# Kernel tuning notes

Hardware: AMD Instinct MI355X
Metric: run time of the kernel (lower is better)

The kernel has to match this reference:

```python
import jax, jax.numpy as jnp
import numpy as np

B, S, E, H = 2, 2048, 1024, 16
HD = E // H


def setup_inputs() -> dict:
    key = jax.random.key(0)
    ks = jax.random.split(key, 5)
    scale = 0.02
    return {
        "x": jax.random.normal(ks[0], (B, S, E), dtype=jnp.float32),
        "qkv_w": jax.random.normal(ks[1], (3 * E, E), dtype=jnp.float32) * scale,
        "qkv_b": jax.random.normal(ks[2], (3 * E,), dtype=jnp.float32) * scale,
        "out_w": jax.random.normal(ks[3], (E, E), dtype=jnp.float32) * scale,
        "out_b": jax.random.normal(ks[4], (E,), dtype=jnp.float32) * scale,
    }


def reference(x, qkv_w, qkv_b, out_w, out_b):
    b, s, e = x.shape
    scale = 1.0 / jnp.sqrt(jnp.float32(HD))
    # fused QKV projection: torch Linear is x @ W.T + b
    qkv = x @ qkv_w.T + qkv_b                       # [b, s, 3e]
    qkv = qkv.reshape(b, s, 3, H, HD)
    qkv = jnp.transpose(qkv, (2, 0, 3, 1, 4))       # [3, b, h, s, hd]
    q, k, v = qkv[0], qkv[1], qkv[2]
    scores = jnp.einsum('bhqd,bhkd->bhqk', q, k) * scale
    # causal mask (atmask=True): mask strictly upper triangle
    causal = jnp.triu(jnp.ones((s, s), dtype=bool), k=1)
    scores = jnp.where(causal, -jnp.inf, scores)
    attn = jax.nn.softmax(scores, axis=-1)          # dropout p=0.0 -> identity
    out = jnp.einsum('bhqk,bhkd->bhqd', attn, v)    # [b, h, s, hd]
    out = jnp.transpose(out, (0, 2, 1, 3)).reshape(b, s, e)
    return out @ out_w.T + out_b
```

## Files before the change

### kernel.cpp

```cpp
#include <hip/hip_runtime.h>
#include <cmath>

typedef __attribute__((ext_vector_type(8))) __bf16 bf16x8;
typedef __attribute__((ext_vector_type(8))) unsigned short ushort8v;
typedef __attribute__((ext_vector_type(4))) float f32x4;

__device__ inline unsigned short f2bf(float f) {
    unsigned int u = __float_as_uint(f);
    unsigned int r = (u + 0x7fffu + ((u >> 16) & 1u)) >> 16;
    return (unsigned short)r;
}

__device__ inline bf16x8 ld8(const unsigned short* p) {
    uint4 v = *(const uint4*)p;
    return __builtin_bit_cast(bf16x8, v);
}

__device__ inline f32x4 mfma16(bf16x8 a, bf16x8 b, f32x4 c) {
    return __builtin_amdgcn_mfma_f32_16x16x32_bf16(a, b, c, 0, 0, 0);
}

__device__ inline unsigned pk2t(float a, float b) {
    return __builtin_amdgcn_perm(__float_as_uint(b), __float_as_uint(a), 0x07060302u);
}

__device__ inline void gl_lds16(const unsigned short* g, const unsigned short* l) {
    __builtin_amdgcn_global_load_lds(
        (const __attribute__((address_space(1))) void*)(unsigned long long)g,
        (__attribute__((address_space(3))) void*)(unsigned)(unsigned long long)l,
        16, 0, 0);
}

#define NX4  1048576
#define NW14 786432
#define NW24 262144
__global__ __launch_bounds__(256) void cvt3(const float* __restrict__ x,
                                            const float* __restrict__ w1,
                                            const float* __restrict__ w2,
                                            unsigned short* __restrict__ xb,
                                            unsigned short* __restrict__ w1b,
                                            unsigned short* __restrict__ w2b) {
    int i = blockIdx.x * 256 + threadIdx.x;
    const float* src;
    unsigned short* dst;
    int off;
    if (i < NX4)              { src = x;  dst = xb;  off = i; }
    else if (i < NX4 + NW14)  { src = w1; dst = w1b; off = i - NX4; }
    else                      { src = w2; dst = w2b; off = i - NX4 - NW14; }
    float4 v = ((const float4*)src)[off];
    ushort4 o;
    o.x = f2bf(v.x); o.y = f2bf(v.y); o.z = f2bf(v.z); o.w = f2bf(v.w);
    ((ushort4*)dst)[off] = o;
}

__global__ __launch_bounds__(256) void gemm_out(const unsigned short* __restrict__ A,
                                                const unsigned short* __restrict__ B,
                                                const float* __restrict__ bias,
                                                float* __restrict__ C,
                                                int M, int N, int K) {
    __shared__ __align__(16) unsigned short As0[64 * 32];
    __shared__ __align__(16) unsigned short Bs0[128 * 32];
    __shared__ __align__(16) unsigned short As1[64 * 32];
    __shared__ __align__(16) unsigned short Bs1[128 * 32];
    const int m0 = blockIdx.y * 64;
    const int n0 = blockIdx.x * 128;
    const int t = threadIdx.x;
    const int wave = t >> 6, lane = t & 63;
    const int l16 = lane & 15, quad = lane >> 4;
    const int wm = (wave >> 1) * 32, wn = (wave & 1) * 64;

    f32x4 acc[2][4] = {};

    const int ra = t >> 2, ka = (t & 3) * 8;
    const int b1 = 256 + t;
    const int rb0 = t >> 2, kb0 = (t & 3) * 8;
    const int rb1 = b1 >> 2, kb1 = (b1 & 3) * 8;

    for (int k0 = 0; k0 < K; k0 += 64) {
        __syncthreads();
        gl_lds16(A + (size_t)(m0 + ra) * K + k0 + ka,        As0 + t * 8);
        gl_lds16(B + (size_t)(n0 + rb0) * K + k0 + kb0,      Bs0 + t * 8);
        gl_lds16(B + (size_t)(n0 + rb1) * K + k0 + kb1,      Bs0 + b1 * 8);
        gl_lds16(A + (size_t)(m0 + ra) * K + k0 + 32 + ka,   As1 + t * 8);
        gl_lds16(B + (size_t)(n0 + rb0) * K + k0 + 32 + kb0, Bs1 + t * 8);
        gl_lds16(B + (size_t)(n0 + rb1) * K + k0 + 32 + kb1, Bs1 + b1 * 8);
        __syncthreads();

        bf16x8 af[2], bfr[4];
        #pragma unroll
        for (int i = 0; i < 2; ++i)
            af[i] = ld8(As0 + (wm + i * 16 + l16) * 32 + quad * 8);
        #pragma unroll
        for (int j = 0; j < 4; ++j)
            bfr[j] = ld8(Bs0 + (wn + j * 16 + l16) * 32 + quad * 8);
        #pragma unroll
        for (int i = 0; i < 2; ++i)
            #pragma unroll
            for (int j = 0; j < 4; ++j)
                acc[i][j] = mfma16(af[i], bfr[j], acc[i][j]);

        #pragma unroll
        for (int i = 0; i < 2; ++i)
            af[i] = ld8(As1 + (wm + i * 16 + l16) * 32 + quad * 8);
        #pragma unroll
        for (int j = 0; j < 4; ++j)
            bfr[j] = ld8(Bs1 + (wn + j * 16 + l16) * 32 + quad * 8);
        #pragma unroll
        for (int i = 0; i < 2; ++i)
            #pragma unroll
            for (int j = 0; j < 4; ++j)
                acc[i][j] = mfma16(af[i], bfr[j], acc[i][j]);
    }

    #pragma unroll
    for (int i = 0; i < 2; ++i) {
        #pragma unroll
        for (int j = 0; j < 4; ++j) {
            int col = n0 + wn + j * 16 + l16;
            float bv = bias[col];
            #pragma unroll
            for (int r = 0; r < 4; ++r) {
                int row = m0 + wm + i * 16 + quad * 4 + r;
                C[(size_t)row * N + col] = acc[i][j][r] + bv;
            }
        }
    }
}

__global__ __launch_bounds__(512, 1) void gemm_qkv(const unsigned short* __restrict__ A,
                                                   const unsigned short* __restrict__ B,
                                                   const float* __restrict__ bias,
                                                   unsigned short* __restrict__ qp,
                                                   unsigned short* __restrict__ kvp,
                                                   int M, int N, int K) {
    __shared__ __align__(16) unsigned short L_[65536];
    const int m0 = blockIdx.y * 256;
    const int n0 = blockIdx.x * 256;
    const int t = threadIdx.x;
    const int wave = t >> 6, lane = t & 63;
    const int l16 = lane & 15, quad = lane >> 4;
    const int wr = wave >> 2, wc = wave & 3;
    const int rswz = (l16 & 7) << 3;

    f32x4 acc[8][4] = {};
    bf16x8 bf[4][2];

    const int c0 = t, c1 = 512 + t;
    const int r0 = c0 >> 3, k0e = ((c0 & 7) ^ (r0 & 7)) * 8;
    const int r1 = c1 >> 3, k1e = ((c1 & 7) ^ (r1 & 7)) * 8;
    const unsigned short* Ab0 = A + (size_t)(m0 + r0) * 1024 + k0e;
    const unsigned short* Ab1 = A + (size_t)(m0 + r1) * 1024 + k1e;
    const unsigned short* Bb0 = B + (size_t)(n0 + r0) * 1024 + k0e;
    const unsigned short* Bb1 = B + (size_t)(n0 + r1) * 1024 + k1e;
    unsigned short* Ld0 = L_ + c0 * 8;
    unsigned short* Ld1 = L_ + c1 * 8;

#define STG_A(par, h, T_) do { \
    gl_lds16(Ab0 + (h) * 131072 + (T_) * 64, Ld0 + (par) * 16384 + (h) * 8192); \
    gl_lds16(Ab1 + (h) * 131072 + (T_) * 64, Ld1 + (par) * 16384 + (h) * 8192); } while (0)
#define STG_B(par, h, T_) do { \
    gl_lds16(Bb0 + (h) * 131072 + (T_) * 64, Ld0 + 32768 + (par) * 16384 + (h) * 8192); \
    gl_lds16(Bb1 + (h) * 131072 + (T_) * 64, Ld1 + 32768 + (par) * 16384 + (h) * 8192); } while (0)

    const unsigned short* Afr = L_ + wr * 8192 + l16 * 64;
    const unsigned short* Bfr = L_ + 32768 + (wc >> 1) * 8192 + ((wc & 1) * 64 + l16) * 64;
    const int koff0 = (quad * 8) ^ rswz;
    const int koff1 = (32 + quad * 8) ^ rswz;

#define LDA0(dst, par, i_) dst = ld8(Afr + (par) * 16384 + (i_) * 1024 + koff0)
#define LDA1(dst, par, i_) dst = ld8(Afr + (par) * 16384 + (i_) * 1024 + koff1)
#define LDB0(dst, par, j_) dst = ld8(Bfr + (par) * 16384 + (j_) * 1024 + koff0)
#define LDB1(dst, par, j_) dst = ld8(Bfr + (par) * 16384 + (j_) * 1024 + koff1)

#define FEN() asm volatile("" ::: "memory")
#define BARR() do { FEN(); __builtin_amdgcn_s_barrier(); FEN(); } while (0)
#define VM4 asm volatile("s_waitcnt vmcnt(4)" ::: "memory")
#define VM0 asm volatile("s_waitcnt vmcnt(0)" ::: "memory")
#define VMN ((void)0)

#define PHASE(PAR, I0, LOADB, STG, VM) do { \
    bf16x8 a00, a01, a10, a11; \
    if (LOADB) { \
        LDB0(bf[0][0], PAR, 0); LDB1(bf[0][1], PAR, 0); \
        LDB0(bf[1][0], PAR, 1); LDB1(bf[1][1], PAR, 1); \
        LDB0(bf[2][0], PAR, 2); LDB1(bf[2][1], PAR, 2); \
        LDB0(bf[3][0], PAR, 3); LDB1(bf[3][1], PAR, 3); \
    } \
    LDA0(a00, PAR, I0); LDA1(a01, PAR, I0); \
    LDA0(a10, PAR, (I0) + 1); LDA1(a11, PAR, (I0) + 1); \
    STG; \
    BARR(); \
    __builtin_amdgcn_s_setprio(1); \
    acc[I0][0] = mfma16(a00, bf[0][0], acc[I0][0]); \
    acc[I0][1] = mfma16(a00, bf[1][0], acc[I0][1]); \
    acc[I0][2] = mfma16(a00, bf[2][0], acc[I0][2]); \
    acc[I0][3] = mfma16(a00, bf[3][0], acc[I0][3]); \
    acc[(I0)+1][0] = mfma16(a10, bf[0][0], acc[(I0)+1][0]); \
    acc[(I0)+1][1] = mfma16(a10, bf[1][0], acc[(I0)+1][1]); \
    acc[(I0)+1][2] = mfma16(a10, bf[2][0], acc[(I0)+1][2]); \
    acc[(I0)+1][3] = mfma16(a10, bf[3][0], acc[(I0)+1][3]); \
    acc[I0][0] = mfma16(a01, bf[0][1], acc[I0][0]); \
    acc[I0][1] = mfma16(a01, bf[1][1], acc[I0][1]); \
    acc[I0][2] = mfma16(a01, bf[2][1], acc[I0][2]); \
    acc[I0][3] = mfma16(a01, bf[3][1], acc[I0][3]); \
    acc[(I0)+1][0] = mfma16(a11, bf[0][1], acc[(I0)+1][0]); \
    acc[(I0)+1][1] = mfma16(a11, bf[1][1], acc[(I0)+1][1]); \
    acc[(I0)+1][2] = mfma16(a11, bf[2][1], acc[(I0)+1][2]); \
    acc[(I0)+1][3] = mfma16(a11, bf[3][1], acc[(I0)+1][3]); \
    __builtin_amdgcn_s_setprio(0); \
    VM; \
    BARR(); \
} while (0)

    STG_A(0, 0, 0); STG_A(0, 1, 0); STG_B(0, 0, 0); STG_B(0, 1, 0);
    STG_B(1, 0, 1); STG_B(1, 1, 1);
    VM4;
    BARR();

    for (int it = 0; it < 7; ++it) {
        const int T = 2 * it;
        PHASE(0, 0, 1, STG_A(1, 0, T + 1), VMN);
        PHASE(0, 2, 0, STG_A(1, 1, T + 1), VMN);
        PHASE(0, 4, 0, STG_B(0, 0, T + 2), VMN);
        PHASE(0, 6, 0, STG_B(0, 1, T + 2), VM4);
        PHASE(1, 0, 1, STG_A(0, 0, T + 2), VMN);
        PHASE(1, 2, 0, STG_A(0, 1, T + 2), VMN);
        PHASE(1, 4, 0, STG_B(1, 0, T + 3), VMN);
        PHASE(1, 6, 0, STG_B(1, 1, T + 3), VM4);
    }
    PHASE(0, 0, 1, STG_A(1, 0, 15), VMN);
    PHASE(0, 2, 0, STG_A(1, 1, 15), VMN);
    PHASE(0, 4, 0, VMN, VMN);
    PHASE(0, 6, 0, VMN, VM0);
    PHASE(1, 0, 1, VMN, VMN);
    PHASE(1, 2, 0, VMN, VMN);
    PHASE(1, 4, 0, VMN, VMN);
    PHASE(1, 6, 0, VMN, VMN);

    __syncthreads();
    const int b = m0 >> 11;

    if (n0 < 1024) {
        const int h0 = n0 >> 6, qt0 = (m0 & 2047) >> 4;
        #pragma unroll
        for (int c = 0; c < 4; ++c) {
            #pragma unroll
            for (int j = 0; j < 4; ++j) {
                float bv = bias[n0 + wc * 64 + j * 16 + l16];
                int half = j >> 1, qd = (j & 1) * 16 + l16;
                int obase = (wc * 4 + wr * 2) * 1024 + half * 512 +
                            (qd >> 3) * 128 + quad * 32 + (qd & 7);
                #pragma unroll
                for (int li = 0; li < 2; ++li) {
                    int ob = obase + li * 1024;
                    #pragma unroll
                    for (int r = 0; r < 4; ++r)
                        L_[ob + r * 8] = f2bf((acc[2 * c + li][j][r] + bv) * 0.180336880f);
                }
            }
            __syncthreads();
            #pragma unroll
            for (int kk = 0; kk < 4; ++kk) {
                int u = t + 512 * kk;
                int unit = u >> 7, within = u & 127;
                int wcp = unit >> 2, slot = unit & 3;
                int qt = qt0 + (slot >> 1) * 8 + c * 2 + (slot & 1);
                int bh = b * 16 + h0 + wcp;
                *(uint4*)(qp + (size_t)(bh * 128 + qt) * 1024 + within * 8) =
                    *(const uint4*)(L_ + u * 8);
            }
            __syncthreads();
        }
    } else if (n0 < 2048) {
        const int h0 = (n0 - 1024) >> 6, tile0 = (m0 & 2047) >> 5;
        const int f2 = (quad & 1) * 2, qh = 4 * (quad >> 1);
        #pragma unroll
        for (int c = 0; c < 4; ++c) {
            #pragma unroll
            for (int j = 0; j < 4; ++j) {
                float bv = bias[n0 + wc * 64 + j * 16 + l16];
                int d = j * 16 + l16;
                int fbit0 = d >> 5, qd = d & 31;
                int obase = (wc * 2 + wr) * 2048 + (f2 | fbit0) * 512 +
                            (qd >> 3) * 128 + qh * 8 + (qd & 7);
                #pragma unroll
                for (int li = 0; li < 2; ++li) {
                    int ob = obase + li * 64;
                    #pragma unroll
                    for (int r = 0; r < 4; ++r)
                        L_[ob + r * 8] = f2bf(acc[2 * c + li][j][r] + bv);
                }
            }
            __syncthreads();
            #pragma unroll
            for (int kk = 0; kk < 4; ++kk) {
                int u = t + 512 * kk;
                int unit = u >> 8, within = u & 255;
                int wcp = unit >> 1, wrp = unit & 1;
                int bh = b * 16 + h0 + wcp;
                int tile = tile0 + wrp * 4 + c;
                *(uint4*)(kvp + (size_t)(bh * 64 + tile) * 4096 + within * 8) =
                    *(const uint4*)(L_ + u * 8);
            }
            __syncthreads();
        }
    } else {
        const int h0 = (n0 - 2048) >> 6, tile0 = (m0 & 2047) >> 5;
        const int kr = quad >> 1, e4 = (quad & 1) * 4;
        #pragma unroll
        for (int c = 0; c < 4; ++c) {
            #pragma unroll
            for (int j = 0; j < 4; ++j) {
                float bv = bias[n0 + wc * 64 + j * 16 + l16];
                int obase = (wc * 2 + wr) * 2048 + j * 512 + (kr * 16 + l16) * 8 + e4;
                #pragma unroll
                for (int li = 0; li < 2; ++li) {
                    int ob = obase + li * 256;
                    unsigned short tmp[4];
                    #pragma unroll
                    for (int r = 0; r < 4; ++r) tmp[r] = f2bf(acc[2 * c + li][j][r] + bv);
                    *(unsigned long long*)(L_ + ob) = *(const unsigned long long*)tmp;
                }
            }
            __syncthreads();
            #pragma unroll
            for (int kk = 0; kk < 4; ++kk) {
                int u = t + 512 * kk;
                int unit = u >> 8, within = u & 255;
                int wcp = unit >> 1, wrp = unit & 1;
                int bh = b * 16 + h0 + wcp;
                int tile = tile0 + wrp * 4 + c;
                *(uint4*)(kvp + (size_t)(bh * 64 + tile) * 4096 + 2048 + within * 8) =
                    *(const uint4*)(L_ + u * 8);
            }
            __syncthreads();
        }
    }
#undef STG_A
#undef STG_B
#undef LDA0
#undef LDA1
#undef LDB0
#undef LDB1
#undef FEN
#undef BARR
#undef VM4
#undef VM0
#undef VMN
#undef PHASE
}

__global__ __launch_bounds__(256, 2) void attn_kernel(const unsigned short* __restrict__ qp,
                                                      const unsigned short* __restrict__ kvp,
                                                      unsigned short* __restrict__ out) {
    const int S = 2048, E = 1024;
    const int wavei = threadIdx.x >> 6;
    const int lane = threadIdx.x & 63;
    const int l16 = lane & 15, quad = lane >> 4;
    const int bidx = blockIdx.x;
    const int bh = (bidx & 7) * 4 + ((bidx >> 3) & 3);
    const int P = 31 - (bidx >> 5);
    const int b = bh >> 4, h = bh & 15;
    const int loff = lane * 8;

    const unsigned short* qbase = qp + (size_t)(bh * 128 + 4 * P) * 1024;
    bf16x8 bq[4][2];
    #pragma unroll
    for (int g = 0; g < 4; ++g) {
        bq[g][0] = ld8(qbase + (2 * g) * 512 + loff);
        bq[g][1] = ld8(qbase + (2 * g + 1) * 512 + loff);
    }

    ushort8v ov;
    #pragma unroll
    for (int j = 0; j < 8; ++j) ov[j] = 0x3F80;
    const bf16x8 ones = __builtin_bit_cast(bf16x8, ov);

    f32x4 O[4][4] = {};
    f32x4 L[4] = {};
    const int nchunks = P + 1;
    const unsigned short* tbase = kvp + (size_t)bh * 64 * 4096;

    for (int c = wavei; c < nchunks; c += 4) {
        const unsigned short* tb = tbase + (size_t)c * 8192;
        bf16x8 f[16];
        #pragma unroll
        for (int i = 0; i < 16; ++i) f[i] = ld8(tb + i * 512 + loff);

        const bool lastc = (c == nchunks - 1);
        const int ks = c * 64;

        #pragma unroll
        for (int tile = 0; tile < 2; ++tile) {
            const bf16x8* g8 = f + tile * 8;
            const int kst = ks + tile * 32;

            f32x4 s0[4], s1[4];
            #pragma unroll
            for (int g = 0; g < 4; ++g) { s0[g] = {}; s1[g] = {}; }
            #pragma unroll
            for (int g = 0; g < 4; ++g) {
                s0[g] = mfma16(g8[0], bq[g][0], s0[g]);
                s0[g] = mfma16(g8[1], bq[g][1], s0[g]);
                s1[g] = mfma16(g8[2], bq[g][0], s1[g]);
                s1[g] = mfma16(g8[3], bq[g][1], s1[g]);
            }

            bf16x8 bp[4];
            #pragma unroll
            for (int g = 0; g < 4; ++g) {
                float p0[4], p1[4];
                if (lastc) {
                    const int qg = 64 * P + 16 * g + l16;
                    #pragma unroll
                    for (int r = 0; r < 4; ++r) {
                        int kk = kst + quad * 8 + r;
                        p0[r] = (kk > qg)     ? 0.f : __builtin_amdgcn_exp2f(s0[g][r]);
                        p1[r] = (kk + 4 > qg) ? 0.f : __builtin_amdgcn_exp2f(s1[g][r]);
                    }
                } else {
                    #pragma unroll
                    for (int r = 0; r < 4; ++r) {
                        p0[r] = __builtin_amdgcn_exp2f(s0[g][r]);
                        p1[r] = __builtin_amdgcn_exp2f(s1[g][r]);
                    }
                }
                uint4 pw;
                pw.x = pk2t(p0[0], p0[1]);
                pw.y = pk2t(p0[2], p0[3]);
                pw.z = pk2t(p1[0], p1[1]);
                pw.w = pk2t(p1[2], p1[3]);
                bp[g] = __builtin_bit_cast(bf16x8, pw);
            }

            #pragma unroll
            for (int g = 0; g < 4; ++g) {
                O[g][0] = mfma16(g8[4], bp[g], O[g][0]);
                O[g][1] = mfma16(g8[5], bp[g], O[g][1]);
                O[g][2] = mfma16(g8[6], bp[g], O[g][2]);
                O[g][3] = mfma16(g8[7], bp[g], O[g][3]);
                L[g]    = mfma16(ones, bp[g], L[g]);
            }
        }
    }

    __shared__ float Ob[4][64][66];
    __shared__ float Lb[4][64];
    #pragma unroll
    for (int g = 0; g < 4; ++g) {
        #pragma unroll
        for (int tn = 0; tn < 4; ++tn)
            #pragma unroll
            for (int r = 0; r < 4; ++r)
                Ob[wavei][g * 16 + l16][tn * 16 + quad * 4 + r] = O[g][tn][r];
        if (quad == 0) Lb[wavei][g * 16 + l16] = L[g][0];
    }
    __syncthreads();

    const int t = threadIdx.x;
    const int qi = t >> 2, hg = (t & 3) * 16;
    float ls = Lb[0][qi] + Lb[1][qi] + Lb[2][qi] + Lb[3][qi];
    const float invl = 1.0f / ls;
    const size_t obase = (size_t)(b * S + 64 * P + qi) * E + h * 64;
    #pragma unroll
    for (int part = 0; part < 2; ++part) {
        int hd0 = hg + part * 8;
        unsigned short o[8];
        #pragma unroll
        for (int k = 0; k < 8; ++k) {
            float a = Ob[0][qi][hd0 + k] + Ob[1][qi][hd0 + k] +
                      Ob[2][qi][hd0 + k] + Ob[3][qi][hd0 + k];
            o[k] = f2bf(a * invl);
        }
        *(uint4*)(out + obase + hd0) = *(uint4*)o;
    }
}

extern "C" void kernel_launch(void* const* d_in, const int* in_sizes, int n_in,
                              void* d_out, int out_size, void* d_ws, size_t ws_size,
                              hipStream_t stream) {
    const float* x     = (const float*)d_in[0];
    const float* qkv_w = (const float*)d_in[1];
    const float* qkv_b = (const float*)d_in[2];
    const float* out_w = (const float*)d_in[3];
    const float* out_b = (const float*)d_in[4];
    float* out = (float*)d_out;

    const int B = 2, S = 2048, E = 1024;
    const int M = B * S;
    const int N1 = 3 * E;

    unsigned short* ws    = (unsigned short*)d_ws;
    unsigned short* xb    = ws;
    unsigned short* w1b   = xb   + (size_t)M * E;
    unsigned short* w2b   = w1b  + (size_t)N1 * E;
    unsigned short* qpb   = w2b  + (size_t)E * E;
    unsigned short* kvpb  = qpb  + (size_t)32 * 128 * 1024;
    unsigned short* attnb = kvpb + (size_t)32 * 64 * 4096;

    cvt3<<<dim3(8192), dim3(256), 0, stream>>>(x, qkv_w, out_w, xb, w1b, w2b);

    gemm_qkv<<<dim3(N1 / 256, M / 256), dim3(512), 0, stream>>>(
        xb, w1b, qkv_b, qpb, kvpb, M, N1, E);

    attn_kernel<<<dim3(1024), dim3(256), 0, stream>>>(qpb, kvpb, attnb);

    gemm_out<<<dim3(E / 128, M / 64), dim3(256), 0, stream>>>(
        attnb, w2b, out_b, out, M, E, E);
}
```

Before: 162.8 us.

## Restructure attention to share double-buffered LDS KV chunks across query-split waves

The attention kernel now gives each block 128 query rows, with each wave owning 32 rows, instead of 64 rows whose KV chunks were split across waves. KV chunks are staged once per block into double-buffered shared memory through global-to-LDS loads, and all four waves read them from there. The cross-wave reduction of partial O and L through shared memory goes away, replaced by a per-wave normalize and store. This halves the grid and is meant to cut redundant global KV traffic, but it adds per-chunk barriers. Waves whose causal range ends early sit idle at those barriers, which creates load imbalance inside the block.

```diff
diff --git a/kernel.cpp b/kernel.cpp
--- a/kernel.cpp
+++ b/kernel.cpp
@@ -350,129 +350,145 @@
 #undef PHASE
 }
 
-__global__ __launch_bounds__(256, 2) void attn_kernel(const unsigned short* __restrict__ qp,
-                                                      const unsigned short* __restrict__ kvp,
-                                                      unsigned short* __restrict__ out) {
+__global__ __launch_bounds__(256) void attn_kernel(const unsigned short* __restrict__ qp,
+                                                   const unsigned short* __restrict__ kvp,
+                                                   unsigned short* __restrict__ out) {
     const int S = 2048, E = 1024;
     const int wavei = threadIdx.x >> 6;
     const int lane = threadIdx.x & 63;
     const int l16 = lane & 15, quad = lane >> 4;
     const int bidx = blockIdx.x;
     const int bh = (bidx & 7) * 4 + ((bidx >> 3) & 3);
-    const int P = 31 - (bidx >> 5);
+    const int p = 15 - (bidx >> 5);
     const int b = bh >> 4, h = bh & 15;
     const int loff = lane * 8;
 
-    const unsigned short* qbase = qp + (size_t)(bh * 128 + 4 * P) * 1024;
-    bf16x8 bq[4][2];
+    const int qt0 = 8 * p + 2 * wavei;
+    const int qrow0 = p * 128 + wavei * 32;
+    const int cmax = (qrow0 + 31) >> 6;
+    const int nch = 2 * p + 2;
+
+    bf16x8 bq[2][2];
     #pragma unroll
-    for (int g = 0; g < 4; ++g) {
-        bq[g][0] = ld8(qbase + (2 * g) * 512 + loff);
-        bq[g][1] = ld8(qbase + (2 * g + 1) * 512 + loff);
-    }
+    for (int g = 0; g < 2; ++g)
+        #pragma unroll
+        for (int hh = 0; hh < 2; ++hh)
+            bq[g][hh] = ld8(qp + (size_t)(bh * 128 + qt0 + g) * 1024 + hh * 512 + loff);
 
     ushort8v ov;
     #pragma unroll
     for (int j = 0; j < 8; ++j) ov[j] = 0x3F80;
     const bf16x8 ones = __builtin_bit_cast(bf16x8, ov);
 
-    f32x4 O[4][4] = {};
-    f32x4 L[4] = {};
-    const int nchunks = P + 1;
-    const unsigned short* tbase = kvp + (size_t)bh * 64 * 4096;
-
-    for (int c = wavei; c < nchunks; c += 4) {
-        const unsigned short* tb = tbase + (size_t)c * 8192;
-        bf16x8 f[16];
-        #pragma unroll
-        for (int i = 0; i < 16; ++i) f[i] = ld8(tb + i * 512 + loff);
-
-        const bool lastc = (c == nchunks - 1);
-        const int ks = c * 64;
-
-        #pragma unroll
-        for (int tile = 0; tile < 2; ++tile) {
-            const bf16x8* g8 = f + tile * 8;
-            const int kst = ks + tile * 32;
-
-            f32x4 s0[4], s1[4];
-            #pragma unroll
-            for (int g = 0; g < 4; ++g) { s0[g] = {}; s1[g] = {}; }
-            #pragma unroll
-            for (int g = 0; g < 4; ++g) {
-                s0[g] = mfma16(g8[0], bq[g][0], s0[g]);
-                s0[g] = mfma16(g8[1], bq[g][1], s0[g]);
-                s1[g] = mfma16(g8[2], bq[g][0], s1[g]);
-                s1[g] = mfma16(g8[3], bq[g][1], s1[g]);
-            }
-
-            bf16x8 bp[4];
-            #pragma unroll
-            for (int g = 0; g < 4; ++g) {
-                float p0[4], p1[4];
-                if (lastc) {
-                    const int qg = 64 * P + 16 * g + l16;
-                    #pragma unroll
-                    for (int r = 0; r < 4; ++r) {
-                        int kk = kst + quad * 8 + r;
-                        p0[r] = (kk > qg)     ? 0.f : __builtin_amdgcn_exp2f(s0[g][r]);
-                        p1[r] = (kk + 4 > qg) ? 0.f : __builtin_amdgcn_exp2f(s1[g][r]);
+    f32x4 O[2][4] = {};
+    f32x4 Lg[2] = {};
+    const unsigned short* tb = kvp + (size_t)bh * 64 * 4096;
+
+    __shared__ __align__(16) unsigned short KV[2][8192];
+
+#define STAGE(C, BUFI) do { \
+    const unsigned short* s_ = tb + (size_t)(C) * 8192; \
+    _Pragma("unroll") \
+    for (int j_ = 0; j_ < 4; ++j_) \
+        gl_lds16(s_ + (threadIdx.x + 256 * j_) * 8, KV[BUFI] + (threadIdx.x + 256 * j_) * 8); \
+} while (0)
+
+    STAGE(0, 0);
+    asm volatile("s_waitcnt vmcnt(0)" ::: "memory");
+    __syncthreads();
+
+    for (int c = 0; c < nch; ++c) {
+        const int cur = c & 1;
+        if (c + 1 < nch) STAGE(c + 1, cur ^ 1);
+        if (c <= cmax) {
+            const unsigned short* cb = KV[cur];
+            const bool maskc = (c == cmax);
+            #pragma unroll
+            for (int tile = 0; tile < 2; ++tile) {
+                const unsigned short* g8 = cb + tile * 4096;
+                const int kst = c * 64 + tile * 32;
+
+                bf16x8 k0 = ld8(g8 + 0 * 512 + loff);
+                bf16x8 k1 = ld8(g8 + 1 * 512 + loff);
+                bf16x8 k2 = ld8(g8 + 2 * 512 + loff);
+                bf16x8 k3 = ld8(g8 + 3 * 512 + loff);
+
+                f32x4 s0[2], s1[2];
+                #pragma unroll
+                for (int g = 0; g < 2; ++g) { s0[g] = {}; s1[g] = {}; }
+                #pragma unroll
+                for (int g = 0; g < 2; ++g) {
+                    s0[g] = mfma16(k0, bq[g][0], s0[g]);
+                    s0[g] = mfma16(k1, bq[g][1], s0[g]);
+                    s1[g] = mfma16(k2, bq[g][0], s1[g]);
+                    s1[g] = mfma16(k3, bq[g][1], s1[g]);
+                }
+
+                bf16x8 bp[2];
+                #pragma unroll
+                for (int g = 0; g < 2; ++g) {
+                    float p0[4], p1[4];
+                    if (maskc) {
+                        const int qg = qrow0 + 16 * g + l16;
+                        #pragma unroll
+                        for (int r = 0; r < 4; ++r) {
+                            int kk = kst + quad * 8 + r;
+                            p0[r] = (kk > qg)     ? 0.f : __builtin_amdgcn_exp2f(s0[g][r]);
+                            p1[r] = (kk + 4 > qg) ? 0.f : __builtin_amdgcn_exp2f(s1[g][r]);
+                        }
+                    } else {
+                        #pragma unroll
+                        for (int r = 0; r < 4; ++r) {
+                            p0[r] = __builtin_amdgcn_exp2f(s0[g][r]);
+                            p1[r] = __builtin_amdgcn_exp2f(s1[g][r]);
+                        }
                     }
-                } else {
-                    #pragma unroll
-                    for (int r = 0; r < 4; ++r) {
-                        p0[r] = __builtin_amdgcn_exp2f(s0[g][r]);
-                        p1[r] = __builtin_amdgcn_exp2f(s1[g][r]);
-                    }
+                    uint4 pw;
+                    pw.x = pk2t(p0[0], p0[1]);
+                    pw.y = pk2t(p0[2], p0[3]);
+                    pw.z = pk2t(p1[0], p1[1]);
+                    pw.w = pk2t(p1[2], p1[3]);
+                    bp[g] = __builtin_bit_cast(bf16x8, pw);
                 }
-                uint4 pw;
-                pw.x = pk2t(p0[0], p0[1]);
-                pw.y = pk2t(p0[2], p0[3]);
-                pw.z = pk2t(p1[0], p1[1]);
-                pw.w = pk2t(p1[2], p1[3]);
-                bp[g] = __builtin_bit_cast(bf16x8, pw);
-            }
-
-            #pragma unroll
-            for (int g = 0; g < 4; ++g) {
-                O[g][0] = mfma16(g8[4], bp[g], O[g][0]);
-                O[g][1] = mfma16(g8[5], bp[g], O[g][1]);
-                O[g][2] = mfma16(g8[6], bp[g], O[g][2]);
-                O[g][3] = mfma16(g8[7], bp[g], O[g][3]);
-                L[g]    = mfma16(ones, bp[g], L[g]);
+
+                bf16x8 v0 = ld8(g8 + 2048 + 0 * 512 + loff);
+                bf16x8 v1 = ld8(g8 + 2048 + 1 * 512 + loff);
+                bf16x8 v2 = ld8(g8 + 2048 + 2 * 512 + loff);
+                bf16x8 v3 = ld8(g8 + 2048 + 3 * 512 + loff);
+                #pragma unroll
+                for (int g = 0; g < 2; ++g) {
+                    O[g][0] = mfma16(v0, bp[g], O[g][0]);
+                    O[g][1] = mfma16(v1, bp[g], O[g][1]);
+                    O[g][2] = mfma16(v2, bp[g], O[g][2]);
+                    O[g][3] = mfma16(v3, bp[g], O[g][3]);
+                    Lg[g]   = mfma16(ones, bp[g], Lg[g]);
+                }
             }
         }
-    }
-
-    __shared__ float Ob[4][64][66];
-    __shared__ float Lb[4][64];
+        __syncthreads();
+    }
+#undef STAGE
+
+    unsigned short* ST = &KV[0][0] + wavei * 2176;
     #pragma unroll
-    for (int g = 0; g < 4; ++g) {
-        #pragma unroll
-        for (int tn = 0; tn < 4; ++tn)
-            #pragma unroll
-            for (int r = 0; r < 4; ++r)
-                Ob[wavei][g * 16 + l16][tn * 16 + quad * 4 + r] = O[g][tn][r];
-        if (quad == 0) Lb[wavei][g * 16 + l16] = L[g][0];
-    }
-    __syncthreads();
-
-    const int t = threadIdx.x;
-    const int qi = t >> 2, hg = (t & 3) * 16;
-    float ls = Lb[0][qi] + Lb[1][qi] + Lb[2][qi] + Lb[3][qi];
-    const float invl = 1.0f / ls;
-    const size_t obase = (size_t)(b * S + 64 * P + qi) * E + h * 64;
+    for (int g = 0; g < 2; ++g) {
+        const float invl = 1.0f / Lg[g][0];
+        #pragma unroll
+        for (int tn = 0; tn < 4; ++tn) {
+            unsigned short tmp[4];
+            #pragma unroll
+            for (int r = 0; r < 4; ++r) tmp[r] = f2bf(O[g][tn][r] * invl);
+            *(unsigned long long*)(ST + (16 * g + l16) * 68 + tn * 16 + quad * 4) =
+                *(const unsigned long long*)tmp;
+        }
+    }
+    const size_t rbase = (size_t)(b * S + p * 128 + wavei * 32) * E + h * 64;
     #pragma unroll
-    for (int part = 0; part < 2; ++part) {
-        int hd0 = hg + part * 8;
-        unsigned short o[8];
-        #pragma unroll
-        for (int k = 0; k < 8; ++k) {
-            float a = Ob[0][qi][hd0 + k] + Ob[1][qi][hd0 + k] +
-                      Ob[2][qi][hd0 + k] + Ob[3][qi][hd0 + k];
-            o[k] = f2bf(a * invl);
-        }
-        *(uint4*)(out + obase + hd0) = *(uint4*)o;
+    for (int it = 0; it < 4; ++it) {
+        int idx = lane + 64 * it;
+        int qq = idx >> 3, dg = idx & 7;
+        *(uint4*)(out + rbase + (size_t)qq * E + dg * 8) =
+            *(const uint4*)(ST + qq * 68 + dg * 8);
     }
 }
 
@@ -503,7 +519,7 @@
     gemm_qkv<<<dim3(N1 / 256, M / 256), dim3(512), 0, stream>>>(
         xb, w1b, qkv_b, qpb, kvpb, M, N1, E);
 
-    attn_kernel<<<dim3(1024), dim3(256), 0, stream>>>(qpb, kvpb, attnb);
+    attn_kernel<<<dim3(512), dim3(256), 0, stream>>>(qpb, kvpb, attnb);
 
     gemm_out<<<dim3(E / 128, M / 64), dim3(256), 0, stream>>>(
         attnb, w2b, out_b, out, M, E, E);
```

Result: slower. 180.6 us (+11.0%).
